# Performance work log

Hardware: AMD Instinct MI355X
Metric: run time of the kernel (lower is better)

The kernel has to match this reference:

```python
import jax, jax.numpy as jnp
import numpy as np

GROUPS = 32
EPS = 1e-5
NUM_HEADS = 16


def group_norm(x, gamma, beta):
    # x: [b, c, s]; GroupNorm over (c//G, s) per group, affine per channel
    b, c, s = x.shape
    xg = x.reshape(b, GROUPS, (c // GROUPS) * s)
    mean = xg.mean(axis=-1, keepdims=True)
    var = xg.var(axis=-1, keepdims=True)
    xn = ((xg - mean) * jax.lax.rsqrt(var + EPS)).reshape(b, c, s)
    return xn * gamma[None, :, None] + beta[None, :, None]


def setup_inputs() -> dict:
    key = jax.random.key(0)
    ks = jax.random.split(key, 8)
    b, c, H, W = 16, 1024, 32, 32
    ctx_dim, Sk = 2048, 256
    x = jax.random.normal(ks[0], (b, c, H, W), jnp.float32)
    context = jax.random.normal(ks[1], (b, Sk, ctx_dim), jnp.float32)
    mask = jax.random.randint(ks[2], (b, Sk), 0, 2, jnp.int32)
    gamma_x = jnp.ones((c,), jnp.float32)
    beta_x = jnp.zeros((c,), jnp.float32)
    gamma_c = jnp.ones((ctx_dim,), jnp.float32)
    beta_c = jnp.zeros((ctx_dim,), jnp.float32)
    Wq = jax.random.normal(ks[3], (c, c), jnp.float32) * (1.0 / np.sqrt(c))
    bq = jnp.zeros((c,), jnp.float32)
    Wkv = jax.random.normal(ks[4], (2 * c, ctx_dim), jnp.float32) * (1.0 / np.sqrt(ctx_dim))
    bkv = jnp.zeros((2 * c,), jnp.float32)
    # proj_out is zero-initialized in the original (zero_module); use small random
    # weights so the attention path contributes to the output / gradients.
    Wp = jax.random.normal(ks[5], (c, c), jnp.float32) * (0.02 / np.sqrt(c))
    bp = jnp.zeros((c,), jnp.float32)
    return {"x": x, "context": context, "mask": mask,
            "gamma_x": gamma_x, "beta_x": beta_x, "gamma_c": gamma_c, "beta_c": beta_c,
            "Wq": Wq, "bq": bq, "Wkv": Wkv, "bkv": bkv, "Wp": Wp, "bp": bp}


def reference(x, context, mask, gamma_x, beta_x, gamma_c, beta_c, Wq, bq, Wkv, bkv, Wp, bp):
    b, c = x.shape[0], x.shape[1]
    spatial = x.shape[2:]
    xf = x.reshape(b, c, -1)                       # [b, c, Sq]
    Sq = xf.shape[-1]
    h_heads = NUM_HEADS
    d = c // h_heads

    # q = conv1x1(GroupNorm(x))
    q = jnp.einsum('oc,bcs->bos', Wq, group_norm(xf, gamma_x, beta_x)) + bq[None, :, None]
    # context -> [b, ctx_dim, Sk], GroupNorm, kv conv1x1
    ctx = jnp.transpose(context, (0, 2, 1))
    ctx_n = group_norm(ctx, gamma_c, beta_c)
    kv = jnp.einsum('oc,bcs->bos', Wkv, ctx_n) + bkv[None, :, None]  # [b, 2c, Sk]
    k, v = kv[:, :c], kv[:, c:]

    # QKVStableMaskedAttention: scale q and k each by 1/sqrt(sqrt(d))
    scale = 1.0 / np.sqrt(np.sqrt(d))
    qh = (q * scale).reshape(b, h_heads, d, Sq)
    kh = (k * scale).reshape(b, h_heads, d, -1)
    vh = v.reshape(b, h_heads, d, -1)
    w = jnp.einsum('bhdt,bhds->bhts', qh, kh)      # [b, h, Sq, Sk]
    mbool = mask.astype(bool)[:, None, None, :]
    w = jnp.where(mbool, w, jnp.float32(-1e9))
    w = jax.nn.softmax(w, axis=-1)                 # stable softmax (max-subtracted)
    a = jnp.einsum('bhts,bhds->bhdt', w, vh).reshape(b, c, Sq)

    h_out = jnp.einsum('oc,bcs->bos', Wp, a) + bp[None, :, None]
    return (xf + h_out).reshape(b, c, *spatial)
```

## Files before the change

kernel.cpp:

```cpp
#include <hip/hip_runtime.h>
#include <stdint.h>

#define DEV static __device__ __forceinline__

typedef unsigned short u16;
typedef u16  u16x8 __attribute__((ext_vector_type(8)));
typedef u16  u16x4 __attribute__((ext_vector_type(4)));
typedef float f32x4 __attribute__((ext_vector_type(4)));
typedef short s16x8 __attribute__((ext_vector_type(8)));

#define BB 16
#define CC 1024
#define SS 1024
#define CTX 2048
#define SKK 256
#define NH 16
#define HD 64
#define NG 32
#define ATT_SCALE 0.35355339059327373f

DEV u16 f2bf(float f) {
  uint32_t u = __float_as_uint(f);
  return (u16)((u + 0x7fffu + ((u >> 16) & 1u)) >> 16);
}
DEV s16x8 ld8(const u16* p) { return __builtin_bit_cast(s16x8, *(const u16x8*)p); }
DEV f32x4 zero4() { f32x4 z = {0.f, 0.f, 0.f, 0.f}; return z; }

DEV void gload_lds16(const void* g, const void* l) {
  __builtin_amdgcn_global_load_lds(
      (const __attribute__((address_space(1))) unsigned int*)(uintptr_t)g,
      (__attribute__((address_space(3))) unsigned int*)(uint32_t)(uintptr_t)l,
      16, 0, 0);
}

__global__ __launch_bounds__(256) void cvt_bf16(const float* __restrict__ in,
                                                u16* __restrict__ out, int n4) {
  int i = blockIdx.x * 256 + threadIdx.x;
  if (i < n4) {
    f32x4 v = ((const f32x4*)in)[i];
    u16x4 o; o[0]=f2bf(v[0]); o[1]=f2bf(v[1]); o[2]=f2bf(v[2]); o[3]=f2bf(v[3]);
    ((u16x4*)out)[i] = o;
  }
}

__global__ __launch_bounds__(256) void gn_stats_x(const float* __restrict__ x,
                                                  float* __restrict__ st) {
  const int b = blockIdx.x >> 5, g = blockIdx.x & 31;
  const float* p = x + ((size_t)b * CC + g * 32) * SS;
  const int tid = threadIdx.x;
  float s = 0.f, ss = 0.f;
  for (int it = 0; it < 32; ++it) {
    f32x4 v = *(const f32x4*)(p + it * 1024 + tid * 4);
    s  += v[0] + v[1] + v[2] + v[3];
    ss += v[0]*v[0] + v[1]*v[1] + v[2]*v[2] + v[3]*v[3];
  }
  __shared__ float red[512];
  red[tid] = s; red[256 + tid] = ss;
  __syncthreads();
  for (int o = 128; o > 0; o >>= 1) {
    if (tid < o) { red[tid] += red[tid + o]; red[256 + tid] += red[256 + tid + o]; }
    __syncthreads();
  }
  if (tid == 0) {
    float mean = red[0] * (1.f / 32768.f);
    float var  = red[256] * (1.f / 32768.f) - mean * mean;
    st[(b * 32 + g) * 2 + 0] = mean;
    st[(b * 32 + g) * 2 + 1] = rsqrtf(var + 1e-5f);
  }
}

__global__ __launch_bounds__(256) void gn_apply_tr_x(const float* __restrict__ x,
                                                     const float* __restrict__ st,
                                                     const float* __restrict__ gamma,
                                                     const float* __restrict__ beta,
                                                     u16* __restrict__ xnT) {
  __shared__ float t[64][65];
  const int b = blockIdx.z, c0 = blockIdx.y * 64, s0 = blockIdx.x * 64;
  const int tid = threadIdx.x, j = tid & 63, i0 = tid >> 6;
  for (int it = 0; it < 16; ++it) {
    int i = it * 4 + i0;
    int c = c0 + i;
    int g = c >> 5;
    float mean = st[(b * 32 + g) * 2], rstd = st[(b * 32 + g) * 2 + 1];
    float v = x[((size_t)b * CC + c) * SS + s0 + j];
    t[i][j] = (v - mean) * rstd * gamma[c] + beta[c];
  }
  __syncthreads();
  for (int it = 0; it < 16; ++it) {
    int jj = it * 4 + i0;
    xnT[((size_t)b * SS + s0 + jj) * CC + c0 + j] = f2bf(t[j][jj]);
  }
}

__global__ __launch_bounds__(256) void gn_stats_c(const float* __restrict__ ctx,
                                                  float* __restrict__ st) {
  const int b = blockIdx.x >> 5, g = blockIdx.x & 31;
  const float* p = ctx + (size_t)b * SKK * CTX + g * 64;
  const int ch = threadIdx.x & 63, r0 = threadIdx.x >> 6;
  float s = 0.f, ss = 0.f;
  for (int it = 0; it < 64; ++it) {
    float v = p[(size_t)(it * 4 + r0) * CTX + ch];
    s += v; ss += v * v;
  }
  __shared__ float red[512];
  const int tid = threadIdx.x;
  red[tid] = s; red[256 + tid] = ss;
  __syncthreads();
  for (int o = 128; o > 0; o >>= 1) {
    if (tid < o) { red[tid] += red[tid + o]; red[256 + tid] += red[256 + tid + o]; }
    __syncthreads();
  }
  if (tid == 0) {
    float mean = red[0] * (1.f / 16384.f);
    float var  = red[256] * (1.f / 16384.f) - mean * mean;
    st[(b * 32 + g) * 2 + 0] = mean;
    st[(b * 32 + g) * 2 + 1] = rsqrtf(var + 1e-5f);
  }
}

__global__ __launch_bounds__(256) void gn_apply_c(const float* __restrict__ ctx,
                                                  const float* __restrict__ st,
                                                  const float* __restrict__ gamma,
                                                  const float* __restrict__ beta,
                                                  u16* __restrict__ out) {
  size_t i = ((size_t)blockIdx.x * 256 + threadIdx.x) * 4;
  int ch = (int)(i & 2047);
  int bs = (int)(i >> 11);
  int b = bs >> 8;
  int g = ch >> 6;
  float mean = st[(b * 32 + g) * 2], rstd = st[(b * 32 + g) * 2 + 1];
  f32x4 v  = *(const f32x4*)(ctx + i);
  f32x4 ga = *(const f32x4*)(gamma + ch);
  f32x4 be = *(const f32x4*)(beta + ch);
  u16x4 o;
  o[0] = f2bf((v[0] - mean) * rstd * ga[0] + be[0]);
  o[1] = f2bf((v[1] - mean) * rstd * ga[1] + be[1]);
  o[2] = f2bf((v[2] - mean) * rstd * ga[2] + be[2]);
  o[3] = f2bf((v[3] - mean) * rstd * ga[3] + be[3]);
  *(u16x4*)(out + i) = o;
}

__global__ __launch_bounds__(256) void mask_bias_k(const int* __restrict__ mask,
                                                   float* __restrict__ mb) {
  int i = blockIdx.x * 256 + threadIdx.x;
  mb[i] = mask[i] ? 0.f : -1e9f;
}

template <int BM, int BN, int EPI>
__global__ __launch_bounds__(256) void gemm_bt(
    const u16* __restrict__ A, const u16* __restrict__ Bt, void* __restrict__ Cout,
    const float* __restrict__ bias, const float* __restrict__ resid,
    int K, int lda, int ldb, int ldc,
    long strideAb, long strideBb, long strideCb, int Nthresh, float scl) {
  constexpr int MF = BM / 32, NF = BN / 32;
  constexpr int ACH = BM / 16, BCH = BN / 16;
  __shared__ alignas(16) u16 lds_a[BM * 32];
  __shared__ alignas(16) u16 lds_b[BN * 32];
  const int tid = threadIdx.x, wid = tid >> 6, lane = tid & 63;
  const int wm = wid >> 1, wn = wid & 1;
  const int b = blockIdx.z;
  const u16* Ab = A + (long)b * strideAb + (long)blockIdx.x * BM * lda;
  const u16* Bb = Bt + (long)b * strideBb + (long)blockIdx.y * BN * ldb;
  const int srow = lane >> 2, scol = (lane & 3) * 8;
  const int fr = lane & 15, fk = (lane >> 4) * 8;

  f32x4 acc[MF][NF];
#pragma unroll
  for (int m = 0; m < MF; ++m)
#pragma unroll
    for (int n = 0; n < NF; ++n) acc[m][n] = zero4();

  for (int kt = 0; kt < K; kt += 32) {
    __syncthreads();
#pragma unroll
    for (int c = 0; c < ACH / 4; ++c) {
      int ch = wid + c * 4;
      gload_lds16(Ab + (long)(ch * 16 + srow) * lda + kt + scol, &lds_a[ch * 512]);
    }
#pragma unroll
    for (int c = 0; c < BCH / 4; ++c) {
      int ch = wid + c * 4;
      gload_lds16(Bb + (long)(ch * 16 + srow) * ldb + kt + scol, &lds_b[ch * 512]);
    }
    __syncthreads();
    s16x8 af[MF], bfr[NF];
#pragma unroll
    for (int m = 0; m < MF; ++m) af[m] = ld8(&lds_a[(wm * (BM / 2) + m * 16 + fr) * 32 + fk]);
#pragma unroll
    for (int n = 0; n < NF; ++n) bfr[n] = ld8(&lds_b[(wn * (BN / 2) + n * 16 + fr) * 32 + fk]);
#pragma unroll
    for (int m = 0; m < MF; ++m)
#pragma unroll
      for (int n = 0; n < NF; ++n)
        acc[m][n] = __builtin_amdgcn_mfma_f32_16x16x32_bf16(af[m], bfr[n], acc[m][n], 0, 0, 0);
  }

  const int rowb = blockIdx.x * BM + wm * (BM / 2) + ((lane >> 4) << 2);
  const int colb = blockIdx.y * BN + wn * (BN / 2) + fr;
#pragma unroll
  for (int m = 0; m < MF; ++m) {
#pragma unroll
    for (int n = 0; n < NF; ++n) {
      int col = colb + n * 16;
      f32x4 v = acc[m][n];
      if constexpr (EPI == 0) {
        float bia = bias[col];
        float s = (col < Nthresh) ? scl : 1.0f;
        u16* C = (u16*)Cout + (long)b * strideCb;
#pragma unroll
        for (int i = 0; i < 4; ++i) {
          int row = rowb + m * 16 + i;
          C[(long)row * ldc + col] = f2bf((v[i] + bia) * s);
        }
      } else {
        float* C = (float*)Cout + (long)b * strideCb;
        const float* R = resid + (long)b * strideCb;
#pragma unroll
        for (int i = 0; i < 4; ++i) {
          int row = rowb + m * 16 + i;
          long idx = (long)row * ldc + col;
          C[idx] = R[idx] + v[i] + bias[row];
        }
      }
    }
  }
}

__global__ __launch_bounds__(256) void transpose_v(const u16* __restrict__ kvt,
                                                   u16* __restrict__ v2) {
  __shared__ u16 t[64][66];
  const int b = blockIdx.z, s0 = blockIdx.y * 64, o0 = blockIdx.x * 64;
  const int tid = threadIdx.x, j = tid & 63, i0 = tid >> 6;
#pragma unroll
  for (int it = 0; it < 16; ++it) {
    int i = it * 4 + i0;
    t[i][j] = kvt[((long)b * SKK + s0 + i) * CTX + CC + o0 + j];
  }
  __syncthreads();
#pragma unroll
  for (int it = 0; it < 16; ++it) {
    int oi = it * 4 + i0;
    v2[((long)b * CC + o0 + oi) * SKK + s0 + j] = t[j][oi];
  }
}

__global__ __launch_bounds__(256) void attn_fused(const u16* __restrict__ qt,
                                                  const u16* __restrict__ kvt,
                                                  const u16* __restrict__ v2,
                                                  const float* __restrict__ mbias,
                                                  u16* __restrict__ at) {
  __shared__ alignas(16) u16 k_lds[256 * 64];
  __shared__ alignas(16) u16 v_lds[64 * 256];
  const int b = blockIdx.z, h = blockIdx.y, t0 = blockIdx.x * 64;
  const int tid = threadIdx.x, wid = tid >> 6, lane = tid & 63;
  const int fr = lane & 15, hi = lane >> 4;
  const int sw = fr & 7;

#pragma unroll
  for (int it = 0; it < 8; ++it) {
    int lin = (wid * 8 + it) * 1024 + lane * 16;
    int kr = lin >> 7, kc = (lin >> 4) & 7;
    gload_lds16(kvt + ((long)b * SKK + kr) * CTX + h * HD + ((kc ^ (kr & 7)) << 3),
                (const char*)k_lds + (wid * 8 + it) * 1024);
    int vr = lin >> 9, vc = (lin >> 4) & 31;
    gload_lds16(v2 + ((long)b * CC + h * HD + vr) * SKK + ((vc ^ (vr & 7)) << 3),
                (const char*)v_lds + (wid * 8 + it) * 1024);
  }

  const u16* qp = qt + ((long)b * SS + t0 + wid * 16 + fr) * CC + h * HD + hi * 8;
  s16x8 aq0 = ld8(qp), aq1 = ld8(qp + 32);

  __syncthreads();

  f32x4 sc[16];
#pragma unroll
  for (int nf = 0; nf < 16; ++nf) {
    const u16* krow = k_lds + (nf * 16 + fr) * 64;
    s16x8 kb0 = ld8(krow + (((hi) ^ sw) << 3));
    s16x8 kb1 = ld8(krow + (((4 + hi) ^ sw) << 3));
    f32x4 z = zero4();
    z = __builtin_amdgcn_mfma_f32_16x16x32_bf16(aq0, kb0, z, 0, 0, 0);
    sc[nf] = __builtin_amdgcn_mfma_f32_16x16x32_bf16(aq1, kb1, z, 0, 0, 0);
  }

  __syncthreads();

  const float* mb = mbias + b * SKK + fr;
#pragma unroll
  for (int nf = 0; nf < 16; ++nf) sc[nf] = sc[nf] + mb[nf * 16];

#pragma unroll
  for (int i = 0; i < 4; ++i) {
    float m = sc[0][i];
#pragma unroll
    for (int nf = 1; nf < 16; ++nf) m = fmaxf(m, sc[nf][i]);
#pragma unroll
    for (int d = 1; d < 16; d <<= 1) m = fmaxf(m, __shfl_xor(m, d));
    float s = 0.f;
#pragma unroll
    for (int nf = 0; nf < 16; ++nf) {
      float e = __expf(sc[nf][i] - m);
      sc[nf][i] = e; s += e;
    }
#pragma unroll
    for (int d = 1; d < 16; d <<= 1) s += __shfl_xor(s, d);
    float inv = 1.0f / s;
#pragma unroll
    for (int nf = 0; nf < 16; ++nf) sc[nf][i] *= inv;
  }

  u16* p_base = k_lds + wid * 4096;
#pragma unroll
  for (int nf = 0; nf < 16; ++nf) {
    int c = 2 * nf + (fr >> 3);
#pragma unroll
    for (int i = 0; i < 4; ++i) {
      int t = 4 * hi + i;
      p_base[t * 256 + (((c ^ (t & 7)) << 3)) + sw] = f2bf(sc[nf][i]);
    }
  }

  f32x4 ov[4];
#pragma unroll
  for (int n = 0; n < 4; ++n) ov[n] = zero4();
#pragma unroll
  for (int kk = 0; kk < 8; ++kk) {
    int c = 4 * kk + hi;
    s16x8 pa = ld8(p_base + fr * 256 + ((c ^ sw) << 3));
#pragma unroll
    for (int n = 0; n < 4; ++n) {
      int o = n * 16 + fr;
      s16x8 vb = ld8(v_lds + o * 256 + ((c ^ sw) << 3));
      ov[n] = __builtin_amdgcn_mfma_f32_16x16x32_bf16(pa, vb, ov[n], 0, 0, 0);
    }
  }

  const int rbase = hi * 4;
  u16* po = at + ((long)b * SS + t0 + wid * 16 + rbase) * CC + h * HD + fr;
#pragma unroll
  for (int n = 0; n < 4; ++n)
#pragma unroll
    for (int i = 0; i < 4; ++i) po[(long)i * CC + n * 16] = f2bf(ov[n][i]);
}

extern "C" void kernel_launch(void* const* d_in, const int* in_sizes, int n_in,
                              void* d_out, int out_size, void* d_ws, size_t ws_size,
                              hipStream_t stream) {
  const float* x       = (const float*)d_in[0];
  const float* context = (const float*)d_in[1];
  const int*   mask    = (const int*)d_in[2];
  const float* gamma_x = (const float*)d_in[3];
  const float* beta_x  = (const float*)d_in[4];
  const float* gamma_c = (const float*)d_in[5];
  const float* beta_c  = (const float*)d_in[6];
  const float* Wq      = (const float*)d_in[7];
  const float* bq      = (const float*)d_in[8];
  const float* Wkv     = (const float*)d_in[9];
  const float* bkv     = (const float*)d_in[10];
  const float* Wp      = (const float*)d_in[11];
  const float* bp      = (const float*)d_in[12];
  float* out = (float*)d_out;

  char* w = (char*)d_ws;
  size_t off = 0;
  u16* wq_bf  = (u16*)(w + off); off += (size_t)CC * CC * 2;
  u16* wkv_bf = (u16*)(w + off); off += (size_t)CTX * CTX * 2;
  u16* wp_bf  = (u16*)(w + off); off += (size_t)CC * CC * 2;
  u16* xnT    = (u16*)(w + off); off += (size_t)BB * SS * CC * 2;
  u16* ctxn   = (u16*)(w + off); off += (size_t)BB * SKK * CTX * 2;
  u16* qt     = (u16*)(w + off); off += (size_t)BB * SS * CC * 2;
  u16* kvt    = (u16*)(w + off); off += (size_t)BB * SKK * CTX * 2;
  u16* v2     = (u16*)(w + off); off += (size_t)BB * CC * SKK * 2;
  u16* at     = (u16*)(w + off); off += (size_t)BB * SS * CC * 2;
  float* mb   = (float*)(w + off); off += (size_t)BB * SKK * 4;
  float* stx  = (float*)(w + off); off += (size_t)BB * NG * 2 * 4;
  float* stc  = (float*)(w + off); off += (size_t)BB * NG * 2 * 4;
  (void)ws_size; (void)in_sizes; (void)n_in; (void)out_size;

  cvt_bf16<<<1024, 256, 0, stream>>>(Wq, wq_bf, CC * CC / 4);
  cvt_bf16<<<4096, 256, 0, stream>>>(Wkv, wkv_bf, CTX * CTX / 4);
  cvt_bf16<<<1024, 256, 0, stream>>>(Wp, wp_bf, CC * CC / 4);

  gn_stats_x<<<512, 256, 0, stream>>>(x, stx);
  gn_apply_tr_x<<<dim3(16, 16, BB), 256, 0, stream>>>(x, stx, gamma_x, beta_x, xnT);
  gn_stats_c<<<512, 256, 0, stream>>>(context, stc);
  gn_apply_c<<<8192, 256, 0, stream>>>(context, stc, gamma_c, beta_c, ctxn);
  mask_bias_k<<<16, 256, 0, stream>>>(mask, mb);

  gemm_bt<128, 128, 0><<<dim3(8, 8, BB), 256, 0, stream>>>(
      xnT, wq_bf, qt, bq, nullptr, CC, CC, CC, CC,
      (long)SS * CC, 0, (long)SS * CC, CC, ATT_SCALE);

  gemm_bt<128, 128, 0><<<dim3(2, 16, BB), 256, 0, stream>>>(
      ctxn, wkv_bf, kvt, bkv, nullptr, CTX, CTX, CTX, CTX,
      (long)SKK * CTX, 0, (long)SKK * CTX, CC, ATT_SCALE);

  transpose_v<<<dim3(16, 4, BB), 256, 0, stream>>>(kvt, v2);

  attn_fused<<<dim3(16, NH, BB), 256, 0, stream>>>(qt, kvt, v2, mb, at);

  gemm_bt<128, 128, 1><<<dim3(8, 8, BB), 256, 0, stream>>>(
      wp_bf, at, out, bp, x, CC, CC, CC, CC,
      0, (long)SS * CC, (long)SS * CC, 0, 1.0f);
}
```

Baseline: 451.5 us.

## Merge prep kernels into fewer launches and remap workgroups across XCDs

Folds the three weight bf16 conversions and the mask-bias kernel into one launch, merges the two GroupNorm stat kernels into one, and merges the two GroupNorm apply kernels into one, cutting the launch count from nine to three. It also remaps the linear workgroup ID in the GEMM and attention kernels so that consecutive logical tiles (same batch or head) land on the same XCD, improving L2 reuse of shared operands. The remap assumes the workgroup count is divisible by 8 and adds some integer division per block.

```diff
diff --git a/kernel.cpp b/kernel.cpp
--- a/kernel.cpp
+++ b/kernel.cpp
@@ -33,26 +33,55 @@
       16, 0, 0);
 }
 
-__global__ __launch_bounds__(256) void cvt_bf16(const float* __restrict__ in,
-                                                u16* __restrict__ out, int n4) {
-  int i = blockIdx.x * 256 + threadIdx.x;
-  if (i < n4) {
-    f32x4 v = ((const f32x4*)in)[i];
-    u16x4 o; o[0]=f2bf(v[0]); o[1]=f2bf(v[1]); o[2]=f2bf(v[2]); o[3]=f2bf(v[3]);
-    ((u16x4*)out)[i] = o;
-  }
-}
-
-__global__ __launch_bounds__(256) void gn_stats_x(const float* __restrict__ x,
-                                                  float* __restrict__ st) {
-  const int b = blockIdx.x >> 5, g = blockIdx.x & 31;
-  const float* p = x + ((size_t)b * CC + g * 32) * SS;
-  const int tid = threadIdx.x;
+__global__ __launch_bounds__(256) void prep_misc(const float* __restrict__ Wq,
+                                                 const float* __restrict__ Wkv,
+                                                 const float* __restrict__ Wp,
+                                                 const int* __restrict__ mask,
+                                                 u16* __restrict__ wq_bf,
+                                                 u16* __restrict__ wkv_bf,
+                                                 u16* __restrict__ wp_bf,
+                                                 float* __restrict__ mb) {
+  const int bid = blockIdx.x, tid = threadIdx.x;
+  const float* src; u16* dst; int i;
+  if (bid < 1024)      { src = Wq;  dst = wq_bf;  i = bid * 256 + tid; }
+  else if (bid < 5120) { src = Wkv; dst = wkv_bf; i = (bid - 1024) * 256 + tid; }
+  else if (bid < 6144) { src = Wp;  dst = wp_bf;  i = (bid - 5120) * 256 + tid; }
+  else {
+    int j = (bid - 6144) * 256 + tid;
+    mb[j] = mask[j] ? 0.f : -1e9f;
+    return;
+  }
+  f32x4 v = ((const f32x4*)src)[i];
+  u16x4 o; o[0]=f2bf(v[0]); o[1]=f2bf(v[1]); o[2]=f2bf(v[2]); o[3]=f2bf(v[3]);
+  ((u16x4*)dst)[i] = o;
+}
+
+__global__ __launch_bounds__(256) void gn_stats_all(const float* __restrict__ x,
+                                                    const float* __restrict__ ctx,
+                                                    float* __restrict__ stx,
+                                                    float* __restrict__ stc) {
+  const int bid = blockIdx.x, tid = threadIdx.x;
   float s = 0.f, ss = 0.f;
-  for (int it = 0; it < 32; ++it) {
-    f32x4 v = *(const f32x4*)(p + it * 1024 + tid * 4);
-    s  += v[0] + v[1] + v[2] + v[3];
-    ss += v[0]*v[0] + v[1]*v[1] + v[2]*v[2] + v[3]*v[3];
+  float* st; int slot; float inv_n;
+  if (bid < 512) {
+    const int b = bid >> 5, g = bid & 31;
+    const float* p = x + ((size_t)b * CC + g * 32) * SS;
+    for (int it = 0; it < 32; ++it) {
+      f32x4 v = *(const f32x4*)(p + it * 1024 + tid * 4);
+      s  += v[0] + v[1] + v[2] + v[3];
+      ss += v[0]*v[0] + v[1]*v[1] + v[2]*v[2] + v[3]*v[3];
+    }
+    st = stx; slot = bid; inv_n = 1.f / 32768.f;
+  } else {
+    const int bid2 = bid - 512;
+    const int b = bid2 >> 5, g = bid2 & 31;
+    const float* p = ctx + (size_t)b * SKK * CTX + g * 64;
+    const int ch = tid & 63, r0 = tid >> 6;
+    for (int it = 0; it < 64; ++it) {
+      float v = p[(size_t)(it * 4 + r0) * CTX + ch];
+      s += v; ss += v * v;
+    }
+    st = stc; slot = bid2; inv_n = 1.f / 16384.f;
   }
   __shared__ float red[512];
   red[tid] = s; red[256 + tid] = ss;
@@ -62,88 +91,59 @@
     __syncthreads();
   }
   if (tid == 0) {
-    float mean = red[0] * (1.f / 32768.f);
-    float var  = red[256] * (1.f / 32768.f) - mean * mean;
-    st[(b * 32 + g) * 2 + 0] = mean;
-    st[(b * 32 + g) * 2 + 1] = rsqrtf(var + 1e-5f);
-  }
-}
-
-__global__ __launch_bounds__(256) void gn_apply_tr_x(const float* __restrict__ x,
-                                                     const float* __restrict__ st,
-                                                     const float* __restrict__ gamma,
-                                                     const float* __restrict__ beta,
-                                                     u16* __restrict__ xnT) {
+    float mean = red[0] * inv_n;
+    float var  = red[256] * inv_n - mean * mean;
+    st[slot * 2 + 0] = mean;
+    st[slot * 2 + 1] = rsqrtf(var + 1e-5f);
+  }
+}
+
+__global__ __launch_bounds__(256) void gn_apply_all(const float* __restrict__ x,
+                                                    const float* __restrict__ ctx,
+                                                    const float* __restrict__ stx,
+                                                    const float* __restrict__ stc,
+                                                    const float* __restrict__ gamma_x,
+                                                    const float* __restrict__ beta_x,
+                                                    const float* __restrict__ gamma_c,
+                                                    const float* __restrict__ beta_c,
+                                                    u16* __restrict__ xnT,
+                                                    u16* __restrict__ ctxn) {
   __shared__ float t[64][65];
-  const int b = blockIdx.z, c0 = blockIdx.y * 64, s0 = blockIdx.x * 64;
-  const int tid = threadIdx.x, j = tid & 63, i0 = tid >> 6;
+  const int bid = blockIdx.x, tid = threadIdx.x;
+  if (bid < 8192) {
+    size_t i = ((size_t)bid * 256 + tid) * 4;
+    int ch = (int)(i & 2047);
+    int bs = (int)(i >> 11);
+    int b = bs >> 8;
+    int g = ch >> 6;
+    float mean = stc[(b * 32 + g) * 2], rstd = stc[(b * 32 + g) * 2 + 1];
+    f32x4 v  = *(const f32x4*)(ctx + i);
+    f32x4 ga = *(const f32x4*)(gamma_c + ch);
+    f32x4 be = *(const f32x4*)(beta_c + ch);
+    u16x4 o;
+    o[0] = f2bf((v[0] - mean) * rstd * ga[0] + be[0]);
+    o[1] = f2bf((v[1] - mean) * rstd * ga[1] + be[1]);
+    o[2] = f2bf((v[2] - mean) * rstd * ga[2] + be[2]);
+    o[3] = f2bf((v[3] - mean) * rstd * ga[3] + be[3]);
+    *(u16x4*)(ctxn + i) = o;
+    return;
+  }
+  const int id2 = bid - 8192;
+  const int b = id2 >> 8, c0 = ((id2 >> 4) & 15) * 64, s0 = (id2 & 15) * 64;
+  const int j = tid & 63, i0 = tid >> 6;
   for (int it = 0; it < 16; ++it) {
     int i = it * 4 + i0;
     int c = c0 + i;
     int g = c >> 5;
-    float mean = st[(b * 32 + g) * 2], rstd = st[(b * 32 + g) * 2 + 1];
+    float mean = stx[(b * 32 + g) * 2], rstd = stx[(b * 32 + g) * 2 + 1];
     float v = x[((size_t)b * CC + c) * SS + s0 + j];
-    t[i][j] = (v - mean) * rstd * gamma[c] + beta[c];
+    t[i][j] = (v - mean) * rstd * gamma_x[c] + beta_x[c];
   }
   __syncthreads();
   for (int it = 0; it < 16; ++it) {
     int jj = it * 4 + i0;
     xnT[((size_t)b * SS + s0 + jj) * CC + c0 + j] = f2bf(t[j][jj]);
   }
-}
-
-__global__ __launch_bounds__(256) void gn_stats_c(const float* __restrict__ ctx,
-                                                  float* __restrict__ st) {
-  const int b = blockIdx.x >> 5, g = blockIdx.x & 31;
-  const float* p = ctx + (size_t)b * SKK * CTX + g * 64;
-  const int ch = threadIdx.x & 63, r0 = threadIdx.x >> 6;
-  float s = 0.f, ss = 0.f;
-  for (int it = 0; it < 64; ++it) {
-    float v = p[(size_t)(it * 4 + r0) * CTX + ch];
-    s += v; ss += v * v;
-  }
-  __shared__ float red[512];
-  const int tid = threadIdx.x;
-  red[tid] = s; red[256 + tid] = ss;
-  __syncthreads();
-  for (int o = 128; o > 0; o >>= 1) {
-    if (tid < o) { red[tid] += red[tid + o]; red[256 + tid] += red[256 + tid + o]; }
-    __syncthreads();
-  }
-  if (tid == 0) {
-    float mean = red[0] * (1.f / 16384.f);
-    float var  = red[256] * (1.f / 16384.f) - mean * mean;
-    st[(b * 32 + g) * 2 + 0] = mean;
-    st[(b * 32 + g) * 2 + 1] = rsqrtf(var + 1e-5f);
-  }
-}
-
-__global__ __launch_bounds__(256) void gn_apply_c(const float* __restrict__ ctx,
-                                                  const float* __restrict__ st,
-                                                  const float* __restrict__ gamma,
-                                                  const float* __restrict__ beta,
-                                                  u16* __restrict__ out) {
-  size_t i = ((size_t)blockIdx.x * 256 + threadIdx.x) * 4;
-  int ch = (int)(i & 2047);
-  int bs = (int)(i >> 11);
-  int b = bs >> 8;
-  int g = ch >> 6;
-  float mean = st[(b * 32 + g) * 2], rstd = st[(b * 32 + g) * 2 + 1];
-  f32x4 v  = *(const f32x4*)(ctx + i);
-  f32x4 ga = *(const f32x4*)(gamma + ch);
-  f32x4 be = *(const f32x4*)(beta + ch);
-  u16x4 o;
-  o[0] = f2bf((v[0] - mean) * rstd * ga[0] + be[0]);
-  o[1] = f2bf((v[1] - mean) * rstd * ga[1] + be[1]);
-  o[2] = f2bf((v[2] - mean) * rstd * ga[2] + be[2]);
-  o[3] = f2bf((v[3] - mean) * rstd * ga[3] + be[3]);
-  *(u16x4*)(out + i) = o;
-}
-
-__global__ __launch_bounds__(256) void mask_bias_k(const int* __restrict__ mask,
-                                                   float* __restrict__ mb) {
-  int i = blockIdx.x * 256 + threadIdx.x;
-  mb[i] = mask[i] ? 0.f : -1e9f;
 }
 
 template <int BM, int BN, int EPI>
@@ -158,9 +158,18 @@
   __shared__ alignas(16) u16 lds_b[BN * 32];
   const int tid = threadIdx.x, wid = tid >> 6, lane = tid & 63;
   const int wm = wid >> 1, wn = wid & 1;
-  const int b = blockIdx.z;
-  const u16* Ab = A + (long)b * strideAb + (long)blockIdx.x * BM * lda;
-  const u16* Bb = Bt + (long)b * strideBb + (long)blockIdx.y * BN * ldb;
+
+  const int nwg  = gridDim.x * gridDim.y * gridDim.z;
+  const int orig = blockIdx.x + gridDim.x * (blockIdx.y + gridDim.y * blockIdx.z);
+  const int v    = (orig & 7) * (nwg >> 3) + (orig >> 3);
+  const int gxy  = gridDim.x * gridDim.y;
+  const int bz   = v / gxy;
+  const int rr   = v - bz * gxy;
+  const int by   = rr / gridDim.x;
+  const int bx   = rr - by * gridDim.x;
+
+  const u16* Ab = A + (long)bz * strideAb + (long)bx * BM * lda;
+  const u16* Bb = Bt + (long)bz * strideBb + (long)by * BN * ldb;
   const int srow = lane >> 2, scol = (lane & 3) * 8;
   const int fr = lane & 15, fk = (lane >> 4) * 8;
 
@@ -195,31 +204,31 @@
         acc[m][n] = __builtin_amdgcn_mfma_f32_16x16x32_bf16(af[m], bfr[n], acc[m][n], 0, 0, 0);
   }
 
-  const int rowb = blockIdx.x * BM + wm * (BM / 2) + ((lane >> 4) << 2);
-  const int colb = blockIdx.y * BN + wn * (BN / 2) + fr;
+  const int rowb = bx * BM + wm * (BM / 2) + ((lane >> 4) << 2);
+  const int colb = by * BN + wn * (BN / 2) + fr;
 #pragma unroll
   for (int m = 0; m < MF; ++m) {
 #pragma unroll
     for (int n = 0; n < NF; ++n) {
       int col = colb + n * 16;
-      f32x4 v = acc[m][n];
+      f32x4 vv = acc[m][n];
       if constexpr (EPI == 0) {
         float bia = bias[col];
         float s = (col < Nthresh) ? scl : 1.0f;
-        u16* C = (u16*)Cout + (long)b * strideCb;
+        u16* C = (u16*)Cout + (long)bz * strideCb;
 #pragma unroll
         for (int i = 0; i < 4; ++i) {
           int row = rowb + m * 16 + i;
-          C[(long)row * ldc + col] = f2bf((v[i] + bia) * s);
+          C[(long)row * ldc + col] = f2bf((vv[i] + bia) * s);
         }
       } else {
-        float* C = (float*)Cout + (long)b * strideCb;
-        const float* R = resid + (long)b * strideCb;
+        float* C = (float*)Cout + (long)bz * strideCb;
+        const float* R = resid + (long)bz * strideCb;
 #pragma unroll
         for (int i = 0; i < 4; ++i) {
           int row = rowb + m * 16 + i;
           long idx = (long)row * ldc + col;
-          C[idx] = R[idx] + v[i] + bias[row];
+          C[idx] = R[idx] + vv[i] + bias[row];
         }
       }
     }
@@ -251,7 +260,10 @@
                                                   u16* __restrict__ at) {
   __shared__ alignas(16) u16 k_lds[256 * 64];
   __shared__ alignas(16) u16 v_lds[64 * 256];
-  const int b = blockIdx.z, h = blockIdx.y, t0 = blockIdx.x * 64;
+  const int orig = blockIdx.x + 16 * blockIdx.y + 256 * blockIdx.z;
+  const int v = (orig & 7) * 512 + (orig >> 3);
+  const int bb = v >> 8, h = (v >> 4) & 15, t0 = (v & 15) * 64;
+
   const int tid = threadIdx.x, wid = tid >> 6, lane = tid & 63;
   const int fr = lane & 15, hi = lane >> 4;
   const int sw = fr & 7;
@@ -260,14 +272,14 @@
   for (int it = 0; it < 8; ++it) {
     int lin = (wid * 8 + it) * 1024 + lane * 16;
     int kr = lin >> 7, kc = (lin >> 4) & 7;
-    gload_lds16(kvt + ((long)b * SKK + kr) * CTX + h * HD + ((kc ^ (kr & 7)) << 3),
+    gload_lds16(kvt + ((long)bb * SKK + kr) * CTX + h * HD + ((kc ^ (kr & 7)) << 3),
                 (const char*)k_lds + (wid * 8 + it) * 1024);
     int vr = lin >> 9, vc = (lin >> 4) & 31;
-    gload_lds16(v2 + ((long)b * CC + h * HD + vr) * SKK + ((vc ^ (vr & 7)) << 3),
+    gload_lds16(v2 + ((long)bb * CC + h * HD + vr) * SKK + ((vc ^ (vr & 7)) << 3),
                 (const char*)v_lds + (wid * 8 + it) * 1024);
   }
 
-  const u16* qp = qt + ((long)b * SS + t0 + wid * 16 + fr) * CC + h * HD + hi * 8;
+  const u16* qp = qt + ((long)bb * SS + t0 + wid * 16 + fr) * CC + h * HD + hi * 8;
   s16x8 aq0 = ld8(qp), aq1 = ld8(qp + 32);
 
   __syncthreads();
@@ -285,7 +297,7 @@
 
   __syncthreads();
 
-  const float* mb = mbias + b * SKK + fr;
+  const float* mb = mbias + bb * SKK + fr;
 #pragma unroll
   for (int nf = 0; nf < 16; ++nf) sc[nf] = sc[nf] + mb[nf * 16];
 
@@ -336,7 +348,7 @@
   }
 
   const int rbase = hi * 4;
-  u16* po = at + ((long)b * SS + t0 + wid * 16 + rbase) * CC + h * HD + fr;
+  u16* po = at + ((long)bb * SS + t0 + wid * 16 + rbase) * CC + h * HD + fr;
 #pragma unroll
   for (int n = 0; n < 4; ++n)
 #pragma unroll
@@ -377,15 +389,13 @@
   float* stc  = (float*)(w + off); off += (size_t)BB * NG * 2 * 4;
   (void)ws_size; (void)in_sizes; (void)n_in; (void)out_size;
 
-  cvt_bf16<<<1024, 256, 0, stream>>>(Wq, wq_bf, CC * CC / 4);
-  cvt_bf16<<<4096, 256, 0, stream>>>(Wkv, wkv_bf, CTX * CTX / 4);
-  cvt_bf16<<<1024, 256, 0, stream>>>(Wp, wp_bf, CC * CC / 4);
-
-  gn_stats_x<<<512, 256, 0, stream>>>(x, stx);
-  gn_apply_tr_x<<<dim3(16, 16, BB), 256, 0, stream>>>(x, stx, gamma_x, beta_x, xnT);
-  gn_stats_c<<<512, 256, 0, stream>>>(context, stc);
-  gn_apply_c<<<8192, 256, 0, stream>>>(context, stc, gamma_c, beta_c, ctxn);
-  mask_bias_k<<<16, 256, 0, stream>>>(mask, mb);
+  prep_misc<<<6160, 256, 0, stream>>>(Wq, Wkv, Wp, mask, wq_bf, wkv_bf, wp_bf, mb);
+
+  gn_stats_all<<<1024, 256, 0, stream>>>(x, context, stx, stc);
+
+  gn_apply_all<<<12288, 256, 0, stream>>>(x, context, stx, stc,
+                                          gamma_x, beta_x, gamma_c, beta_c,
+                                          xnT, ctxn);
 
   gemm_bt<128, 128, 0><<<dim3(8, 8, BB), 256, 0, stream>>>(
       xnT, wq_bf, qt, bq, nullptr, CC, CC, CC, CC,
```

After: 445.8 us. Within noise of the previous version (-1.3%).
